# Kernel tuning notes

Hardware: AMD Instinct MI355X
Metric: run time of the kernel (lower is better)

## Reference

```python
import jax, jax.numpy as jnp
import numpy as np

N_USERS = 50000
N_ITEMS = 75000
N_NODES = N_USERS + N_ITEMS
NNZ = 1250000
EMB = 64
N_LAYERS = 3
BATCH = 4096
EPS = 1e-12


def setup_inputs() -> dict:
    key = jax.random.key(0)
    ks = jax.random.split(key, 12)
    xavier = float(np.sqrt(6.0 / (EMB + EMB)))
    return {
        "user": jax.random.randint(ks[0], (BATCH,), 0, N_USERS, dtype=jnp.int64 if jax.config.jax_enable_x64 else jnp.int32),
        "pos_item": jax.random.randint(ks[1], (BATCH,), 0, N_ITEMS, dtype=jnp.int32),
        "neg_item": jax.random.randint(ks[2], (BATCH,), 0, N_ITEMS, dtype=jnp.int32),
        "row": jax.random.randint(ks[3], (NNZ,), 0, N_NODES, dtype=jnp.int32),
        "col": jax.random.randint(ks[4], (NNZ,), 0, N_NODES, dtype=jnp.int32),
        "vals": jax.random.uniform(ks[5], (NNZ,), dtype=jnp.float32),
        "emb": jax.random.normal(ks[6], (N_NODES, EMB), dtype=jnp.float32) * 0.1,
        "W1": jax.random.uniform(ks[7], (N_LAYERS, EMB, EMB), minval=-xavier, maxval=xavier, dtype=jnp.float32),
        "b1": jnp.zeros((N_LAYERS, EMB), dtype=jnp.float32),
        "W2": jax.random.uniform(ks[8], (N_LAYERS, EMB, EMB), minval=-xavier, maxval=xavier, dtype=jnp.float32),
        "b2": jnp.zeros((N_LAYERS, EMB), dtype=jnp.float32),
    }


def _l2_normalize(x):
    n = jnp.linalg.norm(x, axis=-1, keepdims=True)
    return x / jnp.maximum(n, EPS)


def reference(user, pos_item, neg_item, row, col, vals, emb, W1, b1, W2, b2):
    # eval mode: node_dropout / mess_dropout inactive (rates 0)
    node_feat = emb
    all_embeddings = [node_feat]
    for l in range(N_LAYERS):
        # sparse SpMM: agg[i] = sum_j A[i,j] * node_feat[j]
        msg = vals[:, None] * node_feat[col]            # [nnz, d]
        agg = jax.ops.segment_sum(msg, row, num_segments=N_NODES)  # [N, d]
        part_1 = jax.nn.leaky_relu(agg @ W1[l].T + b1[l], 0.2)
        part_2 = jax.nn.leaky_relu((agg * node_feat) @ W2[l].T + b2[l], 0.2)
        node_feat = part_1 + part_2
        all_embeddings.append(_l2_normalize(node_feat))
    embedding_weight = jnp.concatenate(all_embeddings, axis=-1)  # [N, 4*d]
    gcn_user = embedding_weight[:N_USERS]
    gcn_item = embedding_weight[N_USERS:]
    return (gcn_user[user], gcn_item[pos_item], gcn_item[neg_item])
```

## Files before the change

kernel.cpp:

```cpp
#include <hip/hip_runtime.h>
#include <hip/hip_fp16.h>

#define N_USERS 50000
#define N_ITEMS 75000
#define N_NODES 125000
#define N_PAD   125008
#define NNZ     1250000
#define EMB     64
#define N_LAYERS 3
#define BATCH   4096
#define CONCAT  256

#define BROWS   128
#define NB      ((N_NODES + BROWS - 1) / BROWS)
#define CHUNK   4096
#define NCHUNK  ((NNZ + CHUNK - 1) / CHUNK)
#define EPT     (CHUNK / 256)
#define BCAP    1600
#define FB_NODES 64
#define NT64    ((N_NODES + FB_NODES - 1) / FB_NODES)
#define SCAP    8
#define NCLS    8

#define F4      (N_NODES * EMB / 4)
#define G4      (3 * BATCH * EMB / 4)
#define SM      (3 * BATCH)
#define INIT_ITEMS (F4 + G4 + SM)
#define INIT_BLOCKS ((INIT_ITEMS + 255) / 256)

typedef _Float16 half8  __attribute__((ext_vector_type(8)));
typedef _Float16 half4  __attribute__((ext_vector_type(4)));
typedef float    floatx4 __attribute__((ext_vector_type(4)));

__device__ __forceinline__ bool user_is_i64(const void* uptr) {
    const int* u = (const int*)uptr;
    return (u[1] | u[3] | u[5] | u[7]) == 0;
}
__device__ __forceinline__ int load_user(const void* uptr, int b, bool is64) {
    return is64 ? (int)((const long long*)uptr)[b] : ((const int*)uptr)[b];
}
__device__ __forceinline__ int sample_node(const void* user, const int* pos,
                                           const int* neg, int which, int b,
                                           bool is64) {
    if (which == 0) return load_user(user, b, is64);
    return N_USERS + (which == 1 ? pos[b] : neg[b]);
}

__device__ __forceinline__ float unpack_val(unsigned w) {
    unsigned short us = (unsigned short)(w >> 17);
    _Float16 h = __builtin_bit_cast(_Float16, us);
    return (float)h;
}

__global__ __launch_bounds__(256) void part_init_kernel(
    const int* __restrict__ row, const int* __restrict__ col,
    const float* __restrict__ vals, const float* __restrict__ emb,
    const void* __restrict__ user, const int* __restrict__ pos,
    const int* __restrict__ neg,
    _Float16* __restrict__ f16, float* __restrict__ out,
    int* __restrict__ bcnt, int* __restrict__ scnt, int* __restrict__ smap,
    unsigned long long* __restrict__ sw8) {

    __shared__ int h[NB];
    __shared__ int base[NB];

    if (blockIdx.x < NCHUNK) {
        int t = threadIdx.x;
        int e0 = blockIdx.x * CHUNK;
        int e1 = e0 + CHUNK; if (e1 > NNZ) e1 = NNZ;
        for (int i = t; i < NB; i += 256) h[i] = 0;
        __syncthreads();

        unsigned long long rec[EPT];
        int bkt[EPT];
        int ps[EPT];
        int cnt = 0;
        for (int e = e0 + t; e < e1; e += 256) {
            int r = row[e];
            int b = r >> 7;
            _Float16 hv = (_Float16)vals[e];
            unsigned hb = (unsigned)__builtin_bit_cast(unsigned short, hv);
            rec[cnt] = ((unsigned long long)hb << 24)
                     | ((unsigned)(r & 127) << 17)
                     | (unsigned)col[e];
            bkt[cnt] = b;
            ps[cnt] = atomicAdd(&h[b], 1);
            ++cnt;
        }
        __syncthreads();
        for (int i = t; i < NB; i += 256) {
            int c = h[i];
            if (c) base[i] = atomicAdd(&bcnt[i], c);
        }
        __syncthreads();
        for (int k = 0; k < cnt; ++k) {
            int b = bkt[k];
            sw8[(size_t)b * BCAP + base[b] + ps[k]] = rec[k];
        }
    } else {
        int idx = (blockIdx.x - NCHUNK) * 256 + threadIdx.x;
        bool is64 = user_is_i64(user);
        if (idx < F4) {
            floatx4 v = *(const floatx4*)(emb + (size_t)idx * 4);
            half4 o;
            #pragma unroll
            for (int i = 0; i < 4; ++i) o[i] = (_Float16)v[i];
            *(half4*)(f16 + (size_t)idx * 4) = o;
        } else if (idx < F4 + G4) {
            int j = idx - F4;
            int which = j / (BATCH * 16);
            int rem   = j % (BATCH * 16);
            int bb = rem >> 4, c4 = rem & 15;
            int node = sample_node(user, pos, neg, which, bb, is64);
            floatx4 v = *(const floatx4*)(emb + (size_t)node * EMB + c4 * 4);
            *(floatx4*)(out + (size_t)(which * BATCH + bb) * CONCAT + c4 * 4) = v;
        } else if (idx < F4 + G4 + SM) {
            int g2 = idx - F4 - G4;
            int which = g2 / BATCH, bb = g2 % BATCH;
            int node = sample_node(user, pos, neg, which, bb, is64);
            int slot = atomicAdd(&scnt[node], 1);
            if (slot < SCAP) smap[node * SCAP + slot] = g2;
        }
    }
}

__global__ __launch_bounds__(256) void bucket_sort_kernel(
    const int* __restrict__ bcnt,
    const unsigned long long* __restrict__ sw8,
    unsigned* __restrict__ se, int* __restrict__ off, int* __restrict__ endv,
    int* __restrict__ classcnt) {
    __shared__ unsigned long long ew[BCAP];
    __shared__ unsigned eo[BCAP];
    __shared__ int rh[BROWS], rb[BROWS], rc[BROWS];
    __shared__ int s[256];
    __shared__ int ch[NCLS];

    int b = blockIdx.x, t = threadIdx.x;
    int n = bcnt[b];
    int s0 = b * BCAP;
    if (t < BROWS) rh[t] = 0;
    if (t >= BROWS && t < BROWS + NCLS) ch[t - BROWS] = 0;
    __syncthreads();
    const unsigned long long* src = sw8 + (size_t)b * BCAP;
    for (int i = t; i < n; i += 256) {
        unsigned long long rec = src[i];
        ew[i] = rec;
        atomicAdd(&rh[(int)((rec >> 17) & 127)], 1);
    }
    __syncthreads();
    s[t] = (t < BROWS) ? rh[t] : 0;
    __syncthreads();
    for (int d = 1; d < 256; d <<= 1) {
        int x = (t >= d) ? s[t - d] : 0;
        __syncthreads();
        s[t] += x;
        __syncthreads();
    }
    if (t < BROWS) {
        int excl = s[t] - rh[t];
        rb[t] = excl;
        rc[t] = 0;
        int r = b * BROWS + t;
        if (r < N_NODES) {
            off[r]  = s0 + excl;
            endv[r] = s0 + s[t];
            int c = (rh[t] + 7) >> 3; if (c > NCLS - 1) c = NCLS - 1;
            atomicAdd(&ch[c], 1);
        }
    }
    __syncthreads();
    if (t < NCLS && ch[t]) atomicAdd(&classcnt[t], ch[t]);
    for (int i = t; i < n; i += 256) {
        unsigned long long rec = ew[i];
        int r = (int)((rec >> 17) & 127);
        int p = rb[r] + atomicAdd(&rc[r], 1);
        eo[p] = (unsigned)(((rec >> 24) << 17) | (rec & 0x1FFFFULL));
    }
    __syncthreads();
    for (int i = t; i < n; i += 256)
        se[(size_t)s0 + i] = eo[i];
}

__global__ __launch_bounds__(256) void perm_kernel(
    const int* __restrict__ off, const int* __restrict__ endv,
    const int* __restrict__ classcnt, int* __restrict__ classpos,
    int* __restrict__ perm) {
    __shared__ int lh[NCLS], lbase[NCLS];
    int t = threadIdx.x;
    int node = blockIdx.x * 256 + t;
    if (t < NCLS) lh[t] = 0;
    __syncthreads();
    int c = -1, lpos = 0;
    if (node < N_NODES) {
        int deg = endv[node] - off[node];
        c = (deg + 7) >> 3; if (c > NCLS - 1) c = NCLS - 1;
        lpos = atomicAdd(&lh[c], 1);
    }
    __syncthreads();
    if (t < NCLS) {
        int sbase = 0;
        #pragma unroll
        for (int i = 0; i < NCLS; ++i) if (i < t) sbase += classcnt[i];
        lbase[t] = sbase + (lh[t] ? atomicAdd(&classpos[t], lh[t]) : 0);
    }
    __syncthreads();
    if (node < N_NODES) perm[lbase[c] + lpos] = node;
}

__global__ __launch_bounds__(256) void layer_kernel(
    const int* __restrict__ off, const int* __restrict__ endv,
    const unsigned* __restrict__ se, const int* __restrict__ perm,
    const _Float16* __restrict__ fin, _Float16* __restrict__ fout,
    const float* __restrict__ W1, const float* __restrict__ b1,
    const float* __restrict__ W2, const float* __restrict__ b2,
    const int* __restrict__ scnt, const int* __restrict__ smap,
    float* __restrict__ out, int layer) {

    __shared__ _Float16 wlds[2][EMB][EMB];
    __shared__ _Float16 alds[FB_NODES][EMB];

    int tid = threadIdx.x;

    {
        const float* Wsrc0 = W1 + layer * EMB * EMB;
        const float* Wsrc1 = W2 + layer * EMB * EMB;
        #pragma unroll
        for (int m = 0; m < 2; ++m) {
            const float* Ws = m ? Wsrc1 : Wsrc0;
            for (int c = tid; c < 512; c += 256) {
                int n = c >> 3, c16 = c & 7;
                const float* p = Ws + n * EMB + c16 * 8;
                floatx4 wa = *(const floatx4*)p, wb = *(const floatx4*)(p + 4);
                half8 h;
                #pragma unroll
                for (int i = 0; i < 4; ++i) {
                    h[i] = (_Float16)wa[i]; h[4 + i] = (_Float16)wb[i];
                }
                *(half8*)(&wlds[m][n][(c16 ^ (n & 7)) * 8]) = h;
            }
        }
    }

    int wave = tid >> 6, lane = tid & 63;
    int g = lane >> 3;
    int k = lane & 7;
    int base = blockIdx.x * FB_NODES;
    const _Float16* fink = fin + k * 8;

    for (int p = 0; p < 2; ++p) {
        int ln = p * 32 + wave * 8 + g;
        int idx = base + ln;
        int node = (idx < N_NODES) ? perm[idx] : -1;
        int j = 0, end = 0;
        if (node >= 0) { j = off[node]; end = endv[node]; }

        float acc[8] = {0.f, 0.f, 0.f, 0.f, 0.f, 0.f, 0.f, 0.f};
        while (__any(j < end)) {
            unsigned ev[8];
            #pragma unroll
            for (int t = 0; t < 8; ++t)
                ev[t] = (j + t < end) ? se[j + t] : 0u;
            half8 h[8];
            #pragma unroll
            for (int t = 0; t < 8; ++t) {
                int c = (int)(ev[t] & 0x1FFFFu);
                h[t] = *(const half8*)(fink + (size_t)c * EMB);
            }
            #pragma unroll
            for (int t = 0; t < 8; ++t) {
                float val = unpack_val(ev[t]);
                #pragma unroll
                for (int i = 0; i < 8; ++i)
                    acc[i] += (float)h[t][i] * val;
            }
            j += 8;
        }
        half8 o;
        #pragma unroll
        for (int i = 0; i < 8; ++i) o[i] = (_Float16)acc[i];
        *(half8*)(&alds[ln][(k ^ (ln & 7)) * 8]) = o;
    }
    __syncthreads();

    {
        int lm = lane & 15, quad = lane >> 4;
        int ln0 = wave * 16 + lm;
        int idxD = base + ln0;
        int nodeD = (idxD < N_NODES) ? perm[idxD] : -1;
        int sw = lm & 7;

        half8 a0 = *(const half8*)(&alds[ln0][(quad ^ sw) * 8]);
        half8 a1 = *(const half8*)(&alds[ln0][((quad + 4) ^ sw) * 8]);

        int nsafe = nodeD >= 0 ? nodeD : 0;
        const half8* fp = (const half8*)(fin + (size_t)nsafe * EMB + quad * 8);
        half8 f0 = fp[0], f1 = fp[4];
        half8 g0 = a0 * f0, g1 = a1 * f1;

        float nfv[4][4];
        float sq[4] = {0.f, 0.f, 0.f, 0.f};

        #pragma unroll
        for (int t = 0; t < 4; ++t) {
            int n = t * 16 + lm;
            float bias1 = b1[layer * EMB + n];
            float bias2 = b2[layer * EMB + n];
            half8 w10 = *(const half8*)(&wlds[0][n][(quad ^ sw) * 8]);
            half8 w11 = *(const half8*)(&wlds[0][n][((quad + 4) ^ sw) * 8]);
            half8 w20 = *(const half8*)(&wlds[1][n][(quad ^ sw) * 8]);
            half8 w21 = *(const half8*)(&wlds[1][n][((quad + 4) ^ sw) * 8]);
            floatx4 d1 = {0.f, 0.f, 0.f, 0.f}, d2 = {0.f, 0.f, 0.f, 0.f};
            d1 = __builtin_amdgcn_mfma_f32_16x16x32_f16(a0, w10, d1, 0, 0, 0);
            d1 = __builtin_amdgcn_mfma_f32_16x16x32_f16(a1, w11, d1, 0, 0, 0);
            d2 = __builtin_amdgcn_mfma_f32_16x16x32_f16(g0, w20, d2, 0, 0, 0);
            d2 = __builtin_amdgcn_mfma_f32_16x16x32_f16(g1, w21, d2, 0, 0, 0);
            #pragma unroll
            for (int r = 0; r < 4; ++r) {
                float p1v = d1[r] + bias1;
                p1v = p1v > 0.f ? p1v : 0.2f * p1v;
                float p2v = d2[r] + bias2;
                p2v = p2v > 0.f ? p2v : 0.2f * p2v;
                float nf = p1v + p2v;
                nfv[t][r] = nf;
                sq[r] += nf * nf;
            }
        }

        int nodeO[4];
        #pragma unroll
        for (int r = 0; r < 4; ++r)
            nodeO[r] = __shfl(nodeD, quad * 4 + r, 64);

        if (layer != N_LAYERS - 1) {
            #pragma unroll
            for (int t = 0; t < 4; ++t) {
                int dim = t * 16 + lm;
                #pragma unroll
                for (int r = 0; r < 4; ++r)
                    if (nodeO[r] >= 0)
                        fout[(size_t)nodeO[r] * EMB + dim] = (_Float16)nfv[t][r];
            }
        }

        #pragma unroll
        for (int r = 0; r < 4; ++r) {
            float v = sq[r];
            #pragma unroll
            for (int m = 1; m < 16; m <<= 1) v += __shfl_xor(v, m, 64);
            sq[r] = fmaxf(sqrtf(v), 1e-12f);
        }

        #pragma unroll
        for (int r = 0; r < 4; ++r) {
            if (nodeO[r] < 0) continue;
            int c = scnt[nodeO[r]]; c = c < SCAP ? c : SCAP;
            float inv = 1.0f / sq[r];
            for (int i2 = 0; i2 < c; ++i2) {
                int smp = smap[nodeO[r] * SCAP + i2];
                float* po = out + (size_t)smp * CONCAT + (layer + 1) * EMB;
                #pragma unroll
                for (int t = 0; t < 4; ++t)
                    po[t * 16 + lm] = nfv[t][r] * inv;
            }
        }
    }
}

extern "C" void kernel_launch(void* const* d_in, const int* in_sizes, int n_in,
                              void* d_out, int out_size, void* d_ws, size_t ws_size,
                              hipStream_t stream) {
    const void* user = d_in[0];
    const int* pos  = (const int*)d_in[1];
    const int* neg  = (const int*)d_in[2];
    const int* row  = (const int*)d_in[3];
    const int* col  = (const int*)d_in[4];
    const float* vals = (const float*)d_in[5];
    const float* emb  = (const float*)d_in[6];
    const float* W1   = (const float*)d_in[7];
    const float* b1   = (const float*)d_in[8];
    const float* W2   = (const float*)d_in[9];
    const float* b2   = (const float*)d_in[10];

    _Float16* f16a   = (_Float16*)d_ws;
    _Float16* f16b   = f16a + (size_t)N_PAD * EMB;
    int*      off    = (int*)(f16b + (size_t)N_PAD * EMB);
    int*      endv   = off + (N_NODES + 8);
    int*      perm   = endv + (N_NODES + 8);
    int*      bcnt   = perm + N_NODES;
    int*      scnt   = bcnt + 984;
    int*      classcnt = scnt + N_NODES;
    int*      classpos = classcnt + NCLS;
    int*      smap   = classpos + NCLS;
    unsigned long long* sw8 = (unsigned long long*)(smap + N_NODES * SCAP);
    unsigned* se     = (unsigned*)(sw8 + (size_t)NB * BCAP);

    float* out = (float*)d_out;

    hipMemsetAsync(bcnt, 0, (size_t)(984 + N_NODES + 2 * NCLS) * sizeof(int), stream);

    part_init_kernel<<<NCHUNK + INIT_BLOCKS, 256, 0, stream>>>(
        row, col, vals, emb, user, pos, neg, f16a, out, bcnt, scnt, smap, sw8);

    bucket_sort_kernel<<<NB, 256, 0, stream>>>(bcnt, sw8, se, off, endv, classcnt);

    perm_kernel<<<(N_NODES + 255) / 256, 256, 0, stream>>>(
        off, endv, classcnt, classpos, perm);

    const _Float16* fin = f16a;
    _Float16* fout = f16b;
    for (int l = 0; l < N_LAYERS; ++l) {
        layer_kernel<<<NT64, 256, 0, stream>>>(
            off, endv, se, perm, fin, fout, W1, b1, W2, b2, scnt, smap, out, l);
        const _Float16* tmp = fout; fout = (_Float16*)fin; fin = (const _Float16*)tmp;
    }
}
```

Before: 268.0 us.

## Store permuted CSR offsets and interleave degree-sorted node groups across blocks

```diff
diff --git a/kernel.cpp b/kernel.cpp
--- a/kernel.cpp
+++ b/kernel.cpp
@@ -184,15 +184,16 @@
 __global__ __launch_bounds__(256) void perm_kernel(
     const int* __restrict__ off, const int* __restrict__ endv,
     const int* __restrict__ classcnt, int* __restrict__ classpos,
-    int* __restrict__ perm) {
+    int* __restrict__ perm, int* __restrict__ offp, int* __restrict__ endp) {
     __shared__ int lh[NCLS], lbase[NCLS];
     int t = threadIdx.x;
     int node = blockIdx.x * 256 + t;
     if (t < NCLS) lh[t] = 0;
     __syncthreads();
-    int c = -1, lpos = 0;
+    int c = -1, lpos = 0, o = 0, e = 0;
     if (node < N_NODES) {
-        int deg = endv[node] - off[node];
+        o = off[node]; e = endv[node];
+        int deg = e - o;
         c = (deg + 7) >> 3; if (c > NCLS - 1) c = NCLS - 1;
         lpos = atomicAdd(&lh[c], 1);
     }
@@ -204,11 +205,16 @@
         lbase[t] = sbase + (lh[t] ? atomicAdd(&classpos[t], lh[t]) : 0);
     }
     __syncthreads();
-    if (node < N_NODES) perm[lbase[c] + lpos] = node;
+    if (node < N_NODES) {
+        int d = lbase[c] + lpos;
+        perm[d] = node;
+        offp[d] = o;
+        endp[d] = e;
+    }
 }
 
 __global__ __launch_bounds__(256) void layer_kernel(
-    const int* __restrict__ off, const int* __restrict__ endv,
+    const int* __restrict__ offp, const int* __restrict__ endp,
     const unsigned* __restrict__ se, const int* __restrict__ perm,
     const _Float16* __restrict__ fin, _Float16* __restrict__ fout,
     const float* __restrict__ W1, const float* __restrict__ b1,
@@ -244,15 +250,15 @@
     int wave = tid >> 6, lane = tid & 63;
     int g = lane >> 3;
     int k = lane & 7;
-    int base = blockIdx.x * FB_NODES;
     const _Float16* fink = fin + k * 8;
 
     for (int p = 0; p < 2; ++p) {
-        int ln = p * 32 + wave * 8 + g;
-        int idx = base + ln;
-        int node = (idx < N_NODES) ? perm[idx] : -1;
-        int j = 0, end = 0;
-        if (node >= 0) { j = off[node]; end = endv[node]; }
+        int s = p * 4 + wave;
+        int ln = s * 8 + g;
+        int gi = (s * NT64 + blockIdx.x) * 8 + g;
+        bool v = gi < N_NODES;
+        int j   = v ? offp[gi] : 0;
+        int end = v ? endp[gi] : 0;
 
         float acc[8] = {0.f, 0.f, 0.f, 0.f, 0.f, 0.f, 0.f, 0.f};
         while (__any(j < end)) {
@@ -285,8 +291,9 @@
     {
         int lm = lane & 15, quad = lane >> 4;
         int ln0 = wave * 16 + lm;
-        int idxD = base + ln0;
-        int nodeD = (idxD < N_NODES) ? perm[idxD] : -1;
+        int sD = ln0 >> 3, gD = ln0 & 7;
+        int giD = (sD * NT64 + blockIdx.x) * 8 + gD;
+        int nodeD = (giD < N_NODES) ? perm[giD] : -1;
         int sw = lm & 7;
 
         half8 a0 = *(const half8*)(&alds[ln0][(quad ^ sw) * 8]);
@@ -386,7 +393,9 @@
     int*      off    = (int*)(f16b + (size_t)N_PAD * EMB);
     int*      endv   = off + (N_NODES + 8);
     int*      perm   = endv + (N_NODES + 8);
-    int*      bcnt   = perm + N_NODES;
+    int*      offp   = perm + N_NODES;
+    int*      endp   = offp + (N_NODES + 8);
+    int*      bcnt   = endp + (N_NODES + 8);
     int*      scnt   = bcnt + 984;
     int*      classcnt = scnt + N_NODES;
     int*      classpos = classcnt + NCLS;
@@ -404,13 +413,13 @@
     bucket_sort_kernel<<<NB, 256, 0, stream>>>(bcnt, sw8, se, off, endv, classcnt);
 
     perm_kernel<<<(N_NODES + 255) / 256, 256, 0, stream>>>(
-        off, endv, classcnt, classpos, perm);
+        off, endv, classcnt, classpos, perm, offp, endp);
 
     const _Float16* fin = f16a;
     _Float16* fout = f16b;
     for (int l = 0; l < N_LAYERS; ++l) {
         layer_kernel<<<NT64, 256, 0, stream>>>(
-            off, endv, se, perm, fin, fout, W1, b1, W2, b2, scnt, smap, out, l);
+            offp, endp, se, perm, fin, fout, W1, b1, W2, b2, scnt, smap, out, l);
         const _Float16* tmp = fout; fout = (_Float16*)fin; fin = (const _Float16*)tmp;
     }
 }
```

Measured after the change: 264.3 us. No clear change (-1.4%).
